# Optimization experiments

Hardware: AMD Instinct MI355X
Metric: run time of the kernel (lower is better)

The kernel has to match this reference:

```python
import jax, jax.numpy as jnp
import numpy as np
import math

B, N, M, Lx = 8, 32, 16, 32
D, TE_DIM, IN_DIM, TT = 64, 16, 17, 63   # hid_dim, te_dim, 1+te_dim, hid_dim-1
H, DH, NL = 4, 16, 2
TAU, DELTA = 60.0, 300.0                 # tau, 5 minutes in seconds
P = B * N * M


def _ln(x, g, b):
    mu = x.mean(-1, keepdims=True)
    v = ((x - mu) ** 2).mean(-1, keepdims=True)
    return (x - mu) / jnp.sqrt(v + 1e-5) * g + b


def _time_bias():
    idx = jnp.arange(M)
    dist = jnp.abs(idx[:, None] - idx[None, :]).astype(jnp.float32) * DELTA
    return jnp.log(jnp.exp(-dist / TAU) + 1e-12)


def _pos_enc():
    pos = jnp.arange(M, dtype=jnp.float32)[:, None]
    div = jnp.exp(jnp.arange(0, D, 2, dtype=jnp.float32) * (-math.log(10000.0) / D))
    pe = jnp.zeros((M, D))
    pe = pe.at[:, 0::2].set(jnp.sin(pos * div))
    pe = pe.at[:, 1::2].set(jnp.cos(pos * div))
    return pe


def _heads(t):   # (b, m, D) -> (b, H, m, DH)
    b, m, _ = t.shape
    return t.reshape(b, m, H, DH).transpose(0, 2, 1, 3)


def _merge(t):   # (b, H, m, DH) -> (b, m, D)
    b, _, m, _ = t.shape
    return t.transpose(0, 2, 1, 3).reshape(b, m, D)


def _patch_gattn(x, pm, qw, qb, kw, kb, vw, vb, ow, ob, tbias):
    q, k, v = _heads(x @ qw.T + qb), _heads(x @ kw.T + kb), _heads(x @ vw.T + vb)
    a = jnp.einsum('bhqd,bhkd->bhqk', q, k) / math.sqrt(DH) + tbias[None, None]
    a = jnp.where((pm == 0.0)[:, None, None, :], -1e9, a)
    out = _merge(jnp.einsum('bhqk,bhkd->bhqd', jax.nn.softmax(a, -1), v))
    return (out @ ow.T + ob) * pm[..., None]


def _mha(q_in, kv_in, in_w, in_b, ow, ob, kpm=None):
    wq, wk, wv = in_w[:D], in_w[D:2 * D], in_w[2 * D:]
    bq, bk, bv = in_b[:D], in_b[D:2 * D], in_b[2 * D:]
    q = _heads(q_in @ wq.T + bq)
    k = _heads(kv_in @ wk.T + bk)
    v = _heads(kv_in @ wv.T + bv)
    a = jnp.einsum('bhqd,bhkd->bhqk', q, k) / math.sqrt(DH)
    if kpm is not None:
        a = jnp.where(kpm[:, None, None, :], -1e9, a)
    out = _merge(jnp.einsum('bhqk,bhkd->bhqd', jax.nn.softmax(a, -1), v))
    return out @ ow.T + ob


def _forward(x, mask, ttcn_w1, ttcn_b1, ttcn_w2, ttcn_b2, ttcn_w3, ttcn_b3, t_bias,
             ga_qw, ga_qb, ga_kw, ga_kb, ga_vw, ga_vb, ga_ow, ga_ob,
             tf_in_w, tf_in_b, tf_out_w, tf_out_b, tf_ln1_g, tf_ln1_b, tf_ln2_g, tf_ln2_b,
             tf_fw1, tf_fb1, tf_fw2, tf_fb2,
             q_embed, cls_in_w, cls_in_b, cls_out_w, cls_out_b, logit_w, logit_b):
    m = mask.astype(x.dtype)                          # (P, Lx, 1)
    # --- TTCN: per-sample dynamic filter generation + masked seq-softmax agg ---
    h = jax.nn.relu(x @ ttcn_w1.T + ttcn_b1)
    h = jax.nn.relu(h @ ttcn_w2.T + ttcn_b2)
    filt = h @ ttcn_w3.T + ttcn_b3                    # (P, Lx, IN_DIM*TT)
    filt = filt * m + (1.0 - m) * (-1e8)
    fs = jax.nn.softmax(filt, axis=1).reshape(P, Lx, TT, IN_DIM)
    h_t = jax.nn.relu(jnp.einsum('pli,plti->pt', x, fs) + t_bias)   # (P, TT)
    mask_patch = (m.sum(axis=1) > 0).astype(x.dtype)  # (P, 1)
    xp = jnp.concatenate([h_t, mask_patch], -1).reshape(B, N, M, D)
    pm = mask_patch.reshape(B, N, M)
    tbias = _time_bias()
    pe = _pos_enc()
    xc = xp
    for l in range(NL):
        if l > 0:
            x_last = xc
        xb = xc.reshape(B * N, M, D)
        pmb = pm.reshape(B * N, M)
        xb = xb + _patch_gattn(xb, pmb, ga_qw[l], ga_qb[l], ga_kw[l], ga_kb[l],
                               ga_vw[l], ga_vb[l], ga_ow[l], ga_ob[l], tbias)
        xb = xb + pe[None]
        # post-norm TransformerEncoderLayer (tf_layer = 1, no attn mask, eval mode)
        attn = _mha(xb, xb, tf_in_w[l], tf_in_b[l], tf_out_w[l], tf_out_b[l])
        xb = _ln(xb + attn, tf_ln1_g[l], tf_ln1_b[l])
        ff = jax.nn.relu(xb @ tf_fw1[l].T + tf_fb1[l]) @ tf_fw2[l].T + tf_fb2[l]
        xb = _ln(xb + ff, tf_ln2_g[l], tf_ln2_b[l])
        xc = xb.reshape(B, N, M, D)
        if l > 0:
            xc = x_last + xc
    x_seq = xc.mean(axis=1)                            # (B, M, D)
    kpm = ~((pm > 0).any(axis=1))                      # (B, M), True = padded
    qs = jnp.broadcast_to(q_embed[None], (B, 5, D))
    z = _mha(qs, x_seq, cls_in_w, cls_in_b, cls_out_w, cls_out_b, kpm=kpm)
    return (z @ logit_w.T + logit_b)[..., 0]           # (B, 5)


def setup_inputs() -> dict:
    key = jax.random.key(0)
    ks = iter(jax.random.split(key, 64))
    def rn(shape, s=0.1):
        return jax.random.normal(next(ks), shape, jnp.float32) * s
    inp = {
        'x': jax.random.normal(next(ks), (P, Lx, IN_DIM), jnp.float32),
        'mask': jax.random.randint(next(ks), (P, Lx, 1), 0, 2, jnp.int32),
        'ttcn_w1': rn((TT, IN_DIM)), 'ttcn_b1': jnp.zeros((TT,)),
        'ttcn_w2': rn((TT, TT)), 'ttcn_b2': jnp.zeros((TT,)),
        'ttcn_w3': rn((IN_DIM * TT, TT)), 'ttcn_b3': jnp.zeros((IN_DIM * TT,)),
        't_bias': rn((1, TT)),
        'ga_qw': rn((NL, D, D)), 'ga_qb': jnp.zeros((NL, D)),
        'ga_kw': rn((NL, D, D)), 'ga_kb': jnp.zeros((NL, D)),
        'ga_vw': rn((NL, D, D)), 'ga_vb': jnp.zeros((NL, D)),
        'ga_ow': rn((NL, D, D)), 'ga_ob': jnp.zeros((NL, D)),
        'tf_in_w': rn((NL, 3 * D, D)), 'tf_in_b': jnp.zeros((NL, 3 * D)),
        'tf_out_w': rn((NL, D, D)), 'tf_out_b': jnp.zeros((NL, D)),
        'tf_ln1_g': jnp.ones((NL, D)), 'tf_ln1_b': jnp.zeros((NL, D)),
        'tf_ln2_g': jnp.ones((NL, D)), 'tf_ln2_b': jnp.zeros((NL, D)),
        'tf_fw1': rn((NL, 2048, D)), 'tf_fb1': jnp.zeros((NL, 2048)),
        'tf_fw2': rn((NL, D, 2048)), 'tf_fb2': jnp.zeros((NL, D)),
        'q_embed': rn((5, D), 1.0),
        'cls_in_w': rn((3 * D, D)), 'cls_in_b': jnp.zeros((3 * D,)),
        'cls_out_w': rn((D, D)), 'cls_out_b': jnp.zeros((D,)),
        'logit_w': rn((1, D)), 'logit_b': jnp.zeros((1,)),
    }
    return inp


def reference(x, mask, ttcn_w1, ttcn_b1, ttcn_w2, ttcn_b2, ttcn_w3, ttcn_b3, t_bias,
              ga_qw, ga_qb, ga_kw, ga_kb, ga_vw, ga_vb, ga_ow, ga_ob,
              tf_in_w, tf_in_b, tf_out_w, tf_out_b, tf_ln1_g, tf_ln1_b, tf_ln2_g, tf_ln2_b,
              tf_fw1, tf_fb1, tf_fw2, tf_fb2,
              q_embed, cls_in_w, cls_in_b, cls_out_w, cls_out_b, logit_w, logit_b):
    return _forward(x, mask, ttcn_w1, ttcn_b1, ttcn_w2, ttcn_b2, ttcn_w3, ttcn_b3, t_bias,
                    ga_qw, ga_qb, ga_kw, ga_kb, ga_vw, ga_vb, ga_ow, ga_ob,
                    tf_in_w, tf_in_b, tf_out_w, tf_out_b, tf_ln1_g, tf_ln1_b, tf_ln2_g, tf_ln2_b,
                    tf_fw1, tf_fb1, tf_fw2, tf_fb2,
                    q_embed, cls_in_w, cls_in_b, cls_out_w, cls_out_b, logit_w, logit_b)
```

## Files before the change

### kernel.cpp

```cpp
#include <hip/hip_runtime.h>
#include <hip/hip_bf16.h>
#include <math.h>

#define B_  8
#define N_  32
#define M_  16
#define LX  32
#define D_  64
#define IN_DIM_ 17
#define TT_ 63
#define H_  4
#define DH_ 16
#define P_TOT 4096
#define BN_ 256
#define FF_ 2048

#define FRAG_TOT 83200
#define OFF_INW  2048
#define OFF_OUTW 3584
#define OFF_FW1  4096
#define OFF_FW2  20480

typedef unsigned short ushort_t;
typedef __attribute__((ext_vector_type(8))) short short8;
typedef __attribute__((ext_vector_type(4))) float floatx4;

#define MFMA16(a,b,c) __builtin_amdgcn_mfma_f32_16x16x32_bf16((a),(b),(c),0,0,0)

__device__ __forceinline__ float fast_exp2(float x){
#if __has_builtin(__builtin_amdgcn_exp2f)
  return __builtin_amdgcn_exp2f(x);
#else
  return __expf(x * 0.6931471805599453f);
#endif
}
__device__ __forceinline__ float fast_rcp(float x){
#if __has_builtin(__builtin_amdgcn_rcpf)
  return __builtin_amdgcn_rcpf(x);
#else
  return 1.0f / x;
#endif
}

__device__ __forceinline__ ushort_t f2bf(float f){
  unsigned u = __float_as_uint(f);
  u += 0x7FFFu + ((u >> 16) & 1u);
  return (ushort_t)(u >> 16);
}
__device__ __forceinline__ float bf2f(ushort_t h){ return __uint_as_float(((unsigned)h) << 16); }

__device__ __forceinline__ uint4 pack8(const ushort_t* h){
  uint4 u;
  u.x = (unsigned)h[0] | ((unsigned)h[1] << 16);
  u.y = (unsigned)h[2] | ((unsigned)h[3] << 16);
  u.z = (unsigned)h[4] | ((unsigned)h[5] << 16);
  u.w = (unsigned)h[6] | ((unsigned)h[7] << 16);
  return u;
}

__device__ __forceinline__ void split8(const float* r, short8& hi, short8& lo){
  #pragma unroll
  for (int j = 0; j < 8; ++j){
    float v = r[j];
    ushort_t h = f2bf(v);
    ushort_t l2 = f2bf(v - bf2f(h));
    hi[j] = (short)h; lo[j] = (short)l2;
  }
}
__device__ __forceinline__ uint4 cvt8(const float* r){
  ushort_t hh[8];
  #pragma unroll
  for (int j = 0; j < 8; ++j) hh[j] = f2bf(r[j]);
  return pack8(hh);
}
__device__ __forceinline__ short8 cvt8s(const float* r){
  union { uint4 u4; short8 s8; } cv;
  cv.u4 = cvt8(r);
  return cv.s8;
}

__device__ __forceinline__ floatx4 mm3(short8 ah, short8 al, short8 bh, short8 bl, floatx4 c){
  c = MFMA16(ah, bh, c); c = MFMA16(ah, bl, c); c = MFMA16(al, bh, c); return c;
}

__device__ __forceinline__ float dot64(const float* __restrict__ a, const float* __restrict__ w){
  const float4* a4 = (const float4*)a;
  const float4* w4 = (const float4*)w;
  float acc = 0.f;
  #pragma unroll
  for (int k = 0; k < 16; ++k){ float4 x = a4[k], y = w4[k];
    acc += x.x*y.x + x.y*y.y + x.z*y.z + x.w*y.w; }
  return acc;
}
__device__ __forceinline__ float dot16(const float* __restrict__ a, const float* __restrict__ b){
  const float4* a4 = (const float4*)a; const float4* b4 = (const float4*)b;
  float acc = 0.f;
  #pragma unroll
  for (int k = 0; k < 4; ++k){ float4 x = a4[k], y = b4[k];
    acc += x.x*y.x + x.y*y.y + x.z*y.z + x.w*y.w; }
  return acc;
}

__device__ __forceinline__ void packA68(const float* buf, short8* fA, int tid){
  if (tid < 128){
    int ln = tid & 63, ks = tid >> 6;
    const float* r = buf + (ln & 15)*68 + ks*32 + ((ln >> 4) & 3)*8;
    short8 hi, lo; split8(r, hi, lo);
    fA[tid] = hi; fA[128 + tid] = lo;
  }
}

__device__ __forceinline__ float wsum64(float v){
  v += __shfl_xor(v, 1, 64);  v += __shfl_xor(v, 2, 64);
  v += __shfl_xor(v, 4, 64);  v += __shfl_xor(v, 8, 64);
  v += __shfl_xor(v, 16, 64); v += __shfl_xor(v, 32, 64);
  return v;
}

__global__ __launch_bounds__(256) void prep_kernel(
    const float* __restrict__ w1, const float* __restrict__ w2, const float* __restrict__ w3,
    const float* __restrict__ gqw, const float* __restrict__ gkw,
    const float* __restrict__ gvw, const float* __restrict__ gow,
    const float* __restrict__ inw, const float* __restrict__ outw,
    const float* __restrict__ fw1, const float* __restrict__ fw2,
    uint4* __restrict__ fr)
{
  int s = blockIdx.x*256 + threadIdx.x;
  if (s >= FRAG_TOT) return;
  const float* src; int Nr, Kr, KS, rel; int w3seg = 0, noLo = 0;
  if (s < 256)      { src = w1; Nr=63;  Kr=17; KS=1; rel = s; noLo = 1; }
  else if (s < 768) { src = w2; Nr=63;  Kr=63; KS=2; rel = s-256; noLo = 1; }
  else if (s < 9472){ src = w3; Nr=1071;Kr=63; KS=2; rel = s-768; w3seg = 1; noLo = 1; }
  else {
    int t = s - 9472, l = t / 36864, r2 = t - l*36864;
    if (r2 < 512)        { src = gqw + l*4096;   Nr=64;  Kr=64;   KS=2;  rel = r2; }
    else if (r2 < 1024)  { src = gkw + l*4096;   Nr=64;  Kr=64;   KS=2;  rel = r2-512; }
    else if (r2 < 1536)  { src = gvw + l*4096;   Nr=64;  Kr=64;   KS=2;  rel = r2-1024; }
    else if (r2 < 2048)  { src = gow + l*4096;   Nr=64;  Kr=64;   KS=2;  rel = r2-1536; }
    else if (r2 < 3584)  { src = inw + l*12288;  Nr=192; Kr=64;   KS=2;  rel = r2-2048; }
    else if (r2 < 4096)  { src = outw + l*4096;  Nr=64;  Kr=64;   KS=2;  rel = r2-3584; }
    else if (r2 < 20480) { src = fw1 + l*131072; Nr=2048;Kr=64;   KS=2;  rel = r2-4096; noLo = 1; }
    else                 { src = fw2 + l*131072; Nr=64;  Kr=2048; KS=64; rel = r2-20480; noLo = 1; }
  }
  int lane = rel & 63, tmp = rel >> 6;
  int ks = tmp % KS, nt = tmp / KS;
  int kb = ks*32 + ((lane >> 4) & 3)*8;
  int n, validn;
  if (w3seg){
    int i = nt >> 2, tq = nt & 3;
    int t = tq*16 + (lane & 15);
    n = t*17 + i;
    validn = (t < 63);
  } else {
    n = nt*16 + (lane & 15);
    validn = (n < Nr);
  }
  float v[8];
  #pragma unroll
  for (int j = 0; j < 8; ++j){
    v[j] = (validn && (kb + j) < Kr) ? src[n*Kr + kb + j] : 0.f;
    if (w3seg){
      if ((kb + j) == 63) v[j] = 1.0f;
      v[j] *= 1.4426950408889634f;
    }
  }
  ushort_t hh[8];
  #pragma unroll
  for (int j = 0; j < 8; ++j) hh[j] = f2bf(v[j]);
  fr[s] = pack8(hh);
  if (!noLo){
    ushort_t ll[8];
    #pragma unroll
    for (int j = 0; j < 8; ++j) ll[j] = f2bf(v[j] - bf2f(hh[j]));
    fr[FRAG_TOT + s] = pack8(ll);
  }
}

__global__ __launch_bounds__(256) void ttcn_kernel(
    const float* __restrict__ x, const int* __restrict__ mask,
    const float* __restrict__ b1, const float* __restrict__ b2,
    const float* __restrict__ tb,
    const short8* __restrict__ w1bhi,
    const short8* __restrict__ w2bhi,
    const short8* __restrict__ w3bhi,
    float* __restrict__ xp, float* __restrict__ pm,
    float* __restrict__ xsws)
{
  __shared__ __align__(16) char pool[16512];
  float*    xs    = (float*)(pool + 0);
  float*    xst   = (float*)(pool + 2560);
  int*      cmap  = (int*)  (pool + 5008);
  float*    xsumv = (float*)(pool + 5136);
  int*      Vp    = (int*)  (pool + 5204);
  short8*   xfhi  = (short8*)(pool + 5216);
  ushort_t* h1t   = (ushort_t*)(pool + 7264);
  ushort_t* h2t   = (ushort_t*)(pool + 11872);

  const int p = blockIdx.x, tid = threadIdx.x;
  const int lane = tid & 63, wvi = tid >> 6;
  const int nidx = lane & 15, quad = lane >> 4;

  if (p < 128 && tid < 64) xsws[p*64 + tid] = 0.f;

  for (int idx = tid; idx < LX*IN_DIM_; idx += 256){
    int l = (idx * 3856) >> 16;
    int i = idx - l*17;
    xs[l*20 + i] = x[p*(LX*IN_DIM_) + idx];
  }
  if (tid < 64){
    int mv = (tid < 32) ? mask[p*LX + tid] : 0;
    unsigned long long bal = __ballot(mv != 0);
    if (tid < 32) cmap[tid] = 0;
    int pos = __popcll(bal & ((1ull << tid) - 1ull));
    if (mv != 0) cmap[pos] = tid;
    if (tid == 0) *Vp = (int)__popcll(bal);
  }
  __syncthreads();
  const int V   = *Vp;
  const int two = (V > 16);

  if (tid < 128){
    int mt = tid >> 6;
    if (mt == 0 || two){
      int lc = cmap[mt*16 + nidx];
      float r[8];
      #pragma unroll
      for (int j = 0; j < 8; ++j){
        int k = quad*8 + j;
        r[j] = (k < IN_DIM_) ? xs[lc*20 + k] : 0.f;
      }
      ((uint4*)xfhi)[tid] = cvt8(r);
    }
  } else {
    if (tid < 128 + IN_DIM_){
      int i = tid - 128;
      float s = 0.f;
      #pragma unroll
      for (int l = 0; l < LX; ++l) s += xs[l*20 + i];
      xsumv[i] = s;
    }
    if (two){
      for (int idx = tid - 128; idx < 544; idx += 128){
        int i = idx >> 5, cl = idx & 31;
        xst[i*36 + cl] = xs[cmap[cl]*20 + i];
      }
    } else {
      for (int idx = tid - 128; idx < 272; idx += 128){
        int i = idx >> 4, cl = idx & 15;
        xst[i*36 + cl] = xs[cmap[cl]*20 + i];
      }
    }
  }
  __syncthreads();

  {
    short8 axh0 = xfhi[lane];
    short8 bh = w1bhi[wvi*64 + lane];
    floatx4 a0 = {0.f,0.f,0.f,0.f};
    a0 = MFMA16(axh0, bh, a0);
    int t = wvi*16 + nidx;
    float bb = (t < TT_) ? b1[t] : 0.f;
    if (two){
      short8 axh1 = xfhi[64 + lane];
      floatx4 a1 = {0.f,0.f,0.f,0.f};
      a1 = MFMA16(axh1, bh, a1);
      #pragma unroll
      for (int r = 0; r < 4; ++r)
        h1t[(16+quad*4+r)*72 + t] = f2bf(fmaxf(a1[r] + bb, 0.f));
    }
    #pragma unroll
    for (int r = 0; r < 4; ++r)
      h1t[(quad*4+r)*72 + t] = f2bf(fmaxf(a0[r] + bb, 0.f));
  }
  __syncthreads();

  {
    short8 bh0 = w2bhi[(wvi*2+0)*64 + lane];
    short8 bh1 = w2bhi[(wvi*2+1)*64 + lane];
    short8 a00 = *(const short8*)((const char*)h1t + (nidx*72 + quad*8)*2);
    short8 a01 = *(const short8*)((const char*)h1t + (nidx*72 + 32 + quad*8)*2);
    floatx4 a0 = {0.f,0.f,0.f,0.f};
    a0 = MFMA16(a00, bh0, a0); a0 = MFMA16(a01, bh1, a0);
    int t = wvi*16 + nidx;
    float bb = (t < TT_) ? b2[t] : 0.f;
    if (two){
      short8 a10 = *(const short8*)((const char*)h1t + ((16+nidx)*72 + quad*8)*2);
      short8 a11 = *(const short8*)((const char*)h1t + ((16+nidx)*72 + 32 + quad*8)*2);
      floatx4 a1 = {0.f,0.f,0.f,0.f};
      a1 = MFMA16(a10, bh0, a1); a1 = MFMA16(a11, bh1, a1);
      #pragma unroll
      for (int r = 0; r < 4; ++r)
        h2t[(16+quad*4+r)*72 + t] = f2bf(fmaxf(a1[r] + bb, 0.f));
    }
    #pragma unroll
    for (int r = 0; r < 4; ++r)
      h2t[(quad*4+r)*72 + t] = f2bf(fmaxf(a0[r] + bb, 0.f));
  }
  __syncthreads();

  {
    short8 ah0[2], ah1[2];
    #pragma unroll
    for (int ks = 0; ks < 2; ++ks)
      ah0[ks] = *(const short8*)((const char*)h2t + (nidx*72 + ks*32 + quad*8)*2);
    if (two){
      #pragma unroll
      for (int ks = 0; ks < 2; ++ks)
        ah1[ks] = *(const short8*)((const char*)h2t + ((16+nidx)*72 + ks*32 + quad*8)*2);
    }
    if (quad == 3){
      if (two) ah1[1][7] = (short)((16 + nidx >= V) ? f2bf(-1e8f) : (ushort_t)0);
      else     ah0[1][7] = (short)((nidx >= V)      ? f2bf(-1e8f) : (ushort_t)0);
    }
    const int t_out = wvi*16 + nidx;
    const int rA = quad*4;
    float acc_t = 0.f;
    if (two){
      #pragma unroll
      for (int it = 0; it < 17; ++it){
        short8 bh0 = w3bhi[((wvi + it*4)*2+0)*64 + lane];
        short8 bh1 = w3bhi[((wvi + it*4)*2+1)*64 + lane];
        floatx4 a0 = {0.f,0.f,0.f,0.f}, a1 = {0.f,0.f,0.f,0.f};
        a0 = MFMA16(ah0[0], bh0, a0); a0 = MFMA16(ah0[1], bh1, a0);
        a1 = MFMA16(ah1[0], bh0, a1); a1 = MFMA16(ah1[1], bh1, a1);

        const float4 xA = *(const float4*)(xst + it*36 + rA);
        const float4 xB = *(const float4*)(xst + it*36 + rA + 16);
        float den0 = 0.f, den1 = 0.f, num0 = 0.f, num1 = 0.f;
        float e;
        e = fast_exp2(a0[0]); den0 += e; num0 = fmaf(e, xA.x, num0);
        e = fast_exp2(a0[1]); den0 += e; num0 = fmaf(e, xA.y, num0);
        e = fast_exp2(a0[2]); den0 += e; num0 = fmaf(e, xA.z, num0);
        e = fast_exp2(a0[3]); den0 += e; num0 = fmaf(e, xA.w, num0);
        e = fast_exp2(a1[0]); den1 += e; num1 = fmaf(e, xB.x, num1);
        e = fast_exp2(a1[1]); den1 += e; num1 = fmaf(e, xB.y, num1);
        e = fast_exp2(a1[2]); den1 += e; num1 = fmaf(e, xB.z, num1);
        e = fast_exp2(a1[3]); den1 += e; num1 = fmaf(e, xB.w, num1);
        float den = den0 + den1, num = num0 + num1;
        den += __shfl_xor(den, 16, 64); den += __shfl_xor(den, 32, 64);
        num += __shfl_xor(num, 16, 64); num += __shfl_xor(num, 32, 64);
        float res = (den > 0.f) ? num * fast_rcp(den) : xsumv[it] * (1.f/32.f);
        acc_t += res;
      }
    } else {
      #pragma unroll
      for (int it = 0; it < 17; ++it){
        short8 bh0 = w3bhi[((wvi + it*4)*2+0)*64 + lane];
        short8 bh1 = w3bhi[((wvi + it*4)*2+1)*64 + lane];
        floatx4 a0 = {0.f,0.f,0.f,0.f};
        a0 = MFMA16(ah0[0], bh0, a0); a0 = MFMA16(ah0[1], bh1, a0);

        const float4 xA = *(const float4*)(xst + it*36 + rA);
        float den = 0.f, num = 0.f, e;
        e = fast_exp2(a0[0]); den += e; num = fmaf(e, xA.x, num);
        e = fast_exp2(a0[1]); den += e; num = fmaf(e, xA.y, num);
        e = fast_exp2(a0[2]); den += e; num = fmaf(e, xA.z, num);
        e = fast_exp2(a0[3]); den += e; num = fmaf(e, xA.w, num);
        den += __shfl_xor(den, 16, 64); den += __shfl_xor(den, 32, 64);
        num += __shfl_xor(num, 16, 64); num += __shfl_xor(num, 32, 64);
        float res = (den > 0.f) ? num * fast_rcp(den) : xsumv[it] * (1.f/32.f);
        acc_t += res;
      }
    }
    if (quad == 0 && t_out < TT_)
      xp[p*D_ + t_out] = fmaxf(acc_t + tb[t_out], 0.f);
  }
  if (tid == 0){
    float mp = (V > 0) ? 1.f : 0.f;
    xp[p*D_ + TT_] = mp;
    pm[p] = mp;
  }
}

__global__ __launch_bounds__(512) void layer12_kernel(
    const float* __restrict__ xin, const float* __restrict__ pm,
    const short8* __restrict__ frS,
    const float* __restrict__ gqb, const float* __restrict__ gkb,
    const float* __restrict__ gvb, const float* __restrict__ gob,
    const float* __restrict__ inb, const float* __restrict__ outb,
    const float* __restrict__ ln1g, const float* __restrict__ ln1b,
    const float* __restrict__ fb1, const float* __restrict__ fb2,
    const float* __restrict__ ln2g, const float* __restrict__ ln2b,
    float* __restrict__ xsws)
{
  __shared__ __align__(16) float xb[16*68];
  __shared__ __align__(16) float xb2[16*68];
  __shared__ __align__(16) float q_[16*68];
  __shared__ __align__(16) float k_[16*68];
  __shared__ __align__(16) float v_[16*68];
  __shared__ __align__(16) float ao[16*68];
  __shared__ __align__(16) float ss[1024];
  __shared__ __align__(16) short8 fragA[256];
  __shared__ __align__(16) float hbuf[8*16*36];
  __shared__ __align__(16) float part[8*16*68];
  __shared__ __align__(16) float pe_t[1024];
  __shared__ float tbt[16];
  __shared__ float pmv[16];

  const int bn = blockIdx.x, tid = threadIdx.x;
  const int lane = tid & 63, wvi = tid >> 6;
  const int nidx = lane & 15, quad = lane >> 4;
  const float* xin_p = xin + bn*1024;

  for (int o = tid; o < 1024; o += 512) xb[(o>>6)*68 + (o&63)] = xin_p[o];
  if (tid < 16) pmv[tid] = pm[bn*16 + tid];
  for (int o = tid; o < 1024; o += 512){
    int tok = o >> 6, d = o & 63;
    float div = __expf((float)(d & ~1) * (-0.14391156831212793f));
    float arg = (float)tok * div;
    pe_t[o] = (d & 1) ? cosf(arg) : sinf(arg);
  }
  if (tid >= 32 && tid < 48) tbt[tid-32] = logf(expf(-5.0f*(float)(tid-32)) + 1e-12f);
  __syncthreads();

  for (int l = 0; l < 2; ++l){
    const int lbase = 9472 + l*36864;
    const float* gqbL = gqb + l*64;  const float* gkbL = gkb + l*64;
    const float* gvbL = gvb + l*64;  const float* gobL = gob + l*64;
    const float* inbL = inb + l*192; const float* outbL = outb + l*64;
    const float* ln1gL = ln1g + l*64; const float* ln1bL = ln1b + l*64;
    const float* fb1L = fb1 + l*2048; const float* fb2L = fb2 + l*64;
    const float* ln2gL = ln2g + l*64; const float* ln2bL = ln2b + l*64;

    float xres[2];
    xres[0] = xb[wvi*68 + lane];
    xres[1] = xb[(wvi+8)*68 + lane];

    short8 gU0[4], gU1[4], mU0[4], mU1[4], ob4[4];
    {
      int b0 = lbase + wvi*128;
      gU0[0] = frS[b0 + lane];       gU0[1] = frS[FRAG_TOT + b0 + lane];
      gU0[2] = frS[b0 + 64 + lane];  gU0[3] = frS[FRAG_TOT + b0 + 64 + lane];
      int m0 = lbase + OFF_INW + wvi*128;
      mU0[0] = frS[m0 + lane];       mU0[1] = frS[FRAG_TOT + m0 + lane];
      mU0[2] = frS[m0 + 64 + lane];  mU0[3] = frS[FRAG_TOT + m0 + 64 + lane];
      if (wvi < 4){
        int b1 = lbase + (wvi+8)*128;
        gU1[0] = frS[b1 + lane];       gU1[1] = frS[FRAG_TOT + b1 + lane];
        gU1[2] = frS[b1 + 64 + lane];  gU1[3] = frS[FRAG_TOT + b1 + 64 + lane];
        int m1 = lbase + OFF_INW + (wvi+8)*128;
        mU1[0] = frS[m1 + lane];       mU1[1] = frS[FRAG_TOT + m1 + lane];
        mU1[2] = frS[m1 + 64 + lane];  mU1[3] = frS[FRAG_TOT + m1 + 64 + lane];
        int bo = lbase + 1536 + wvi*128;
        ob4[0] = frS[bo + lane];       ob4[1] = frS[FRAG_TOT + bo + lane];
        ob4[2] = frS[bo + 64 + lane];  ob4[3] = frS[FRAG_TOT + bo + 64 + lane];
      }
    }

    packA68(xb, fragA, tid);
    __syncthreads();
    {
      short8 axh0 = fragA[lane], axh1 = fragA[64+lane];
      short8 axl0 = fragA[128+lane], axl1 = fragA[192+lane];
      {
        int u = wvi;
        floatx4 c = {0.f,0.f,0.f,0.f};
        c = mm3(axh0, axl0, gU0[0], gU0[1], c);
        c = mm3(axh1, axl1, gU0[2], gU0[3], c);
        int sel = u >> 2, d = (u & 3)*16 + nidx;
        float bb = (sel == 0 ? gqbL : gkbL)[d];
        float* dst = (sel == 0 ? q_ : k_);
        #pragma unroll
        for (int r = 0; r < 4; ++r) dst[(quad*4+r)*68 + d] = c[r] + bb;
      }
      if (wvi < 4){
        int u = wvi + 8;
        floatx4 c = {0.f,0.f,0.f,0.f};
        c = mm3(axh0, axl0, gU1[0], gU1[1], c);
        c = mm3(axh1, axl1, gU1[2], gU1[3], c);
        int d = (u & 3)*16 + nidx;
        float bb = gvbL[d];
        #pragma unroll
        for (int r = 0; r < 4; ++r) v_[(quad*4+r)*68 + d] = c[r] + bb;
      }
    }
    __syncthreads();
    {
      int row = tid >> 3;
      int h = row >> 4, qm = row & 15;
      int km0 = (tid & 7) * 2;
      float s2[2];
      #pragma unroll
      for (int j = 0; j < 2; ++j){
        int km = km0 + j;
        float acc = dot16(q_ + qm*68 + h*16, k_ + km*68 + h*16);
        int dd = qm - km; if (dd < 0) dd = -dd;
        acc = acc * 0.25f + tbt[dd];
        if (pmv[km] == 0.f) acc = -1e9f;
        s2[j] = acc;
      }
      float mx = fmaxf(s2[0], s2[1]);
      mx = fmaxf(mx, __shfl_xor(mx, 1, 64));
      mx = fmaxf(mx, __shfl_xor(mx, 2, 64));
      mx = fmaxf(mx, __shfl_xor(mx, 4, 64));
      float e2[2], se = 0.f;
      #pragma unroll
      for (int j = 0; j < 2; ++j){ e2[j] = __expf(s2[j]-mx); se += e2[j]; }
      se += __shfl_xor(se, 1, 64);
      se += __shfl_xor(se, 2, 64);
      se += __shfl_xor(se, 4, 64);
      float inv = fast_rcp(se);
      #pragma unroll
      for (int j = 0; j < 2; ++j) ss[row*16 + km0 + j] = e2[j]*inv;
    }
    __syncthreads();
    for (int o = tid; o < 1024; o += 512){
      int m = o >> 6, d = o & 63, h = d >> 4;
      float acc = 0.f;
      #pragma unroll
      for (int km = 0; km < 16; ++km) acc += ss[h*256 + m*16 + km] * v_[km*68 + d];
      ao[m*68 + d] = acc;
    }
    __syncthreads();
    packA68(ao, fragA, tid);
    __syncthreads();
    if (wvi < 4){
      short8 axh0 = fragA[lane], axh1 = fragA[64+lane];
      short8 axl0 = fragA[128+lane], axl1 = fragA[192+lane];
      floatx4 c = {0.f,0.f,0.f,0.f};
      c = mm3(axh0, axl0, ob4[0], ob4[1], c);
      c = mm3(axh1, axl1, ob4[2], ob4[3], c);
      int d = wvi*16 + nidx;
      float bb = gobL[d];
      #pragma unroll
      for (int r = 0; r < 4; ++r){
        int tok = quad*4 + r;
        xb[tok*68 + d] += (c[r] + bb) * pmv[tok] + pe_t[tok*64 + d];
      }
    }
    __syncthreads();

    short8 mob[4], f1c[4], f2c[4];
    if (wvi < 4){
      int base = lbase + OFF_OUTW + wvi*128;
      mob[0] = frS[base + lane];       mob[1] = frS[FRAG_TOT + base + lane];
      mob[2] = frS[base + 64 + lane];  mob[3] = frS[FRAG_TOT + base + 64 + lane];
    }
    {
      int f1base = lbase + OFF_FW1, f2base = lbase + OFF_FW2;
      #pragma unroll
      for (int t2 = 0; t2 < 2; ++t2){
        int sb = f1base + ((wvi*16+t2)*2)*64 + lane;
        f1c[t2*2+0] = frS[sb];
        f1c[t2*2+1] = frS[sb + 64];
      }
      #pragma unroll
      for (int ntd = 0; ntd < 4; ++ntd)
        f2c[ntd] = frS[f2base + (ntd*64 + wvi*8)*64 + lane];
    }

    packA68(xb, fragA, tid);
    __syncthreads();
    {
      short8 axh0 = fragA[lane], axh1 = fragA[64+lane];
      short8 axl0 = fragA[128+lane], axl1 = fragA[192+lane];
      {
        int u = wvi;
        floatx4 c = {0.f,0.f,0.f,0.f};
        c = mm3(axh0, axl0, mU0[0], mU0[1], c);
        c = mm3(axh1, axl1, mU0[2], mU0[3], c);
        int sel = u >> 2, d = (u & 3)*16 + nidx;
        float bb = inbL[u*16 + nidx];
        float* dst = (sel == 0 ? q_ : k_);
        #pragma unroll
        for (int r = 0; r < 4; ++r) dst[(quad*4+r)*68 + d] = c[r] + bb;
      }
      if (wvi < 4){
        int u = wvi + 8;
        floatx4 c = {0.f,0.f,0.f,0.f};
        c = mm3(axh0, axl0, mU1[0], mU1[1], c);
        c = mm3(axh1, axl1, mU1[2], mU1[3], c);
        int d = (u & 3)*16 + nidx;
        float bb = inbL[u*16 + nidx];
        #pragma unroll
        for (int r = 0; r < 4; ++r) v_[(quad*4+r)*68 + d] = c[r] + bb;
      }
    }
    __syncthreads();
    {
      int row = tid >> 3;
      int h = row >> 4, qm = row & 15;
      int km0 = (tid & 7) * 2;
      float s2[2];
      #pragma unroll
      for (int j = 0; j < 2; ++j)
        s2[j] = 0.25f * dot16(q_ + qm*68 + h*16, k_ + (km0+j)*68 + h*16);
      float mx = fmaxf(s2[0], s2[1]);
      mx = fmaxf(mx, __shfl_xor(mx, 1, 64));
      mx = fmaxf(mx, __shfl_xor(mx, 2, 64));
      mx = fmaxf(mx, __shfl_xor(mx, 4, 64));
      float e2[2], se = 0.f;
      #pragma unroll
      for (int j = 0; j < 2; ++j){ e2[j] = __expf(s2[j]-mx); se += e2[j]; }
      se += __shfl_xor(se, 1, 64);
      se += __shfl_xor(se, 2, 64);
      se += __shfl_xor(se, 4, 64);
      float inv = fast_rcp(se);
      #pragma unroll
      for (int j = 0; j < 2; ++j) ss[row*16 + km0 + j] = e2[j]*inv;
    }
    __syncthreads();
    for (int o = tid; o < 1024; o += 512){
      int m = o >> 6, d = o & 63, h = d >> 4;
      float acc = 0.f;
      #pragma unroll
      for (int km = 0; km < 16; ++km) acc += ss[h*256 + m*16 + km] * v_[km*68 + d];
      ao[m*68 + d] = acc;
    }
    __syncthreads();
    packA68(ao, fragA, tid);
    __syncthreads();
    if (wvi < 4){
      short8 axh0 = fragA[lane], axh1 = fragA[64+lane];
      short8 axl0 = fragA[128+lane], axl1 = fragA[192+lane];
      floatx4 c = {0.f,0.f,0.f,0.f};
      c = mm3(axh0, axl0, mob[0], mob[1], c);
      c = mm3(axh1, axl1, mob[2], mob[3], c);
      int d = wvi*16 + nidx;
      float bb = outbL[d];
      #pragma unroll
      for (int r = 0; r < 4; ++r) xb[(quad*4+r)*68 + d] += c[r] + bb;
    }
    __syncthreads();

    {
      float a = xb[wvi*68 + lane], b = xb[(wvi+8)*68 + lane];
      float mua = wsum64(a) * (1.f/64.f);
      float mub = wsum64(b) * (1.f/64.f);
      float da = a - mua, db = b - mub;
      float va = wsum64(da*da) * (1.f/64.f);
      float vb = wsum64(db*db) * (1.f/64.f);
      float rva = rsqrtf(va + 1e-5f), rvb = rsqrtf(vb + 1e-5f);
      float g = ln1gL[lane], bia = ln1bL[lane];
      xb2[wvi*68 + lane]     = da*rva*g + bia;
      xb2[(wvi+8)*68 + lane] = db*rvb*g + bia;
    }
    __syncthreads();
    packA68(xb2, fragA, tid);
    __syncthreads();

    {
      const int w = wvi;
      const int f1base = lbase + OFF_FW1, f2base = lbase + OFF_FW2;
      short8 axh0 = fragA[lane], axh1 = fragA[64 + lane];
      floatx4 y0 = {0.f,0.f,0.f,0.f}, y1 = y0, y2 = y0, y3 = y0;
      float* hw = hbuf + w*576;

      short8 f1n[4], f2n[4];
      for (int it = 0; it < 8; ++it){
        int ntA = w*16 + it*2;
        floatx4 hA = {0.f,0.f,0.f,0.f}, hB = hA;
        hA = MFMA16(axh0, f1c[0], hA); hA = MFMA16(axh1, f1c[1], hA);
        hB = MFMA16(axh0, f1c[2], hB); hB = MFMA16(axh1, f1c[3], hB);
        float bbA = fb1L[ntA*16 + nidx], bbB = fb1L[ntA*16 + 16 + nidx];
        #pragma unroll
        for (int r = 0; r < 4; ++r){
          hw[(quad*4+r)*36 + nidx]      = fmaxf(hA[r] + bbA, 0.f);
          hw[(quad*4+r)*36 + 16 + nidx] = fmaxf(hB[r] + bbB, 0.f);
        }
        if (it < 7){
          int ntN = ntA + 2, kstN = w*8 + it + 1;
          #pragma unroll
          for (int t2 = 0; t2 < 2; ++t2){
            int sb = f1base + ((ntN+t2)*2)*64 + lane;
            f1n[t2*2+0] = frS[sb];
            f1n[t2*2+1] = frS[sb + 64];
          }
          #pragma unroll
          for (int ntd = 0; ntd < 4; ++ntd)
            f2n[ntd] = frS[f2base + (ntd*64 + kstN)*64 + lane];
        }
        short8 ah = cvt8s(hw + (lane & 15)*36 + quad*8);
        y0 = MFMA16(ah, f2c[0], y0);
        y1 = MFMA16(ah, f2c[1], y1);
        y2 = MFMA16(ah, f2c[2], y2);
        y3 = MFMA16(ah, f2c[3], y3);
        #pragma unroll
        for (int j = 0; j < 4; ++j){ f1c[j] = f1n[j]; f2c[j] = f2n[j]; }
      }
      #pragma unroll
      for (int r = 0; r < 4; ++r){
        int row = (quad*4 + r)*68;
        part[w*1088 + row + nidx]      = y0[r];
        part[w*1088 + row + 16 + nidx] = y1[r];
        part[w*1088 + row + 32 + nidx] = y2[r];
        part[w*1088 + row + 48 + nidx] = y3[r];
      }
    }
    __syncthreads();
    {
      float ra = xb2[wvi*68 + lane] + fb2L[lane];
      float rb = xb2[(wvi+8)*68 + lane] + fb2L[lane];
      #pragma unroll
      for (int ww = 0; ww < 8; ++ww){
        ra += part[ww*1088 + wvi*68 + lane];
        rb += part[ww*1088 + (wvi+8)*68 + lane];
      }
      float mua = wsum64(ra) * (1.f/64.f);
      float mub = wsum64(rb) * (1.f/64.f);
      float da = ra - mua, db = rb - mub;
      float va = wsum64(da*da) * (1.f/64.f);
      float vb = wsum64(db*db) * (1.f/64.f);
      float rva = rsqrtf(va + 1e-5f), rvb = rsqrtf(vb + 1e-5f);
      float g = ln2gL[lane], bia = ln2bL[lane];
      float vva = da*rva*g + bia;
      float vvb = db*rvb*g + bia;
      if (l == 0){
        xb[wvi*68 + lane]     = vva;
        xb[(wvi+8)*68 + lane] = vvb;
      } else {
        int b = bn >> 5;
        atomicAdd(&xsws[(b*M_ + wvi)*64 + lane],     (vva + xres[0]) * (1.f/32.f));
        atomicAdd(&xsws[(b*M_ + wvi + 8)*64 + lane], (vvb + xres[1]) * (1.f/32.f));
      }
    }
    __syncthreads();
  }
}

__global__ __launch_bounds__(256) void final_kernel(
    const float* __restrict__ xsws, const float* __restrict__ pm,
    const float* __restrict__ q_embed,
    const float* __restrict__ cin_w, const float* __restrict__ cin_b,
    const float* __restrict__ cout_w, const float* __restrict__ cout_b,
    const float* __restrict__ logit_w, const float* __restrict__ logit_b,
    float* __restrict__ out)
{
  const int b = blockIdx.x;
  const int tid = threadIdx.x;
  __shared__ __align__(16) float xs[M_ * D_];
  __shared__ float kpmv[M_];
  __shared__ __align__(16) float qv[5 * D_], kv[M_ * D_], vv[M_ * D_];
  __shared__ float sv[H_ * 5 * M_];
  __shared__ __align__(16) float ao[5 * D_], zv[5 * D_];

  for (int o = tid; o < M_ * D_; o += 256) xs[o] = xsws[b*M_*D_ + o];
  if (tid < M_) {
    float any = 0.f;
    #pragma unroll
    for (int n = 0; n < N_; ++n) any += (pm[(b * N_ + n) * M_ + tid] > 0.f) ? 1.f : 0.f;
    kpmv[tid] = (any > 0.f) ? 0.f : 1.f;
  }
  __syncthreads();

  for (int o = tid; o < 5 * D_; o += 256) {
    int qi = o >> 6, d = o & 63;
    qv[o] = cin_b[d] + dot64(q_embed + qi * D_, cin_w + d * D_);
  }
  for (int o = tid; o < 2 * M_ * D_; o += 256) {
    int sel = o >> 10, r = o & 1023, m = r >> 6, d = r & 63;
    float acc = cin_b[D_ + sel * D_ + d] + dot64(xs + m * D_, cin_w + (D_ + sel * D_ + d) * D_);
    ((sel == 0) ? kv : vv)[r] = acc;
  }
  __syncthreads();

  for (int o = tid; o < H_ * 5 * M_; o += 256) {
    int h = o / 80, r = o % 80, qi = r >> 4, km = r & 15;
    float acc = 0.25f * dot16(qv + qi * D_ + h * DH_, kv + km * D_ + h * DH_);
    if (kpmv[km] != 0.f) acc = -1e9f;
    sv[o] = acc;
  }
  __syncthreads();
  if (tid < H_ * 5) {
    int h = tid / 5, qi = tid % 5;
    float* row = sv + h * 80 + qi * M_;
    float mx = -1e30f;
    #pragma unroll
    for (int km = 0; km < M_; ++km) mx = fmaxf(mx, row[km]);
    float se = 0.f;
    #pragma unroll
    for (int km = 0; km < M_; ++km) { float e = __expf(row[km] - mx); row[km] = e; se += e; }
    float inv = 1.f / se;
    #pragma unroll
    for (int km = 0; km < M_; ++km) row[km] *= inv;
  }
  __syncthreads();
  for (int o = tid; o < 5 * D_; o += 256) {
    int qi = o >> 6, d = o & 63, h = d >> 4;
    float acc = 0.f;
    #pragma unroll
    for (int km = 0; km < M_; ++km) acc += sv[h * 80 + qi * M_ + km] * vv[km * D_ + d];
    ao[o] = acc;
  }
  __syncthreads();
  for (int o = tid; o < 5 * D_; o += 256) {
    int qi = o >> 6, d = o & 63;
    zv[o] = cout_b[d] + dot64(ao + qi * D_, cout_w + d * D_);
  }
  __syncthreads();
  if (tid < 5) {
    float acc = logit_b[0] + dot64(zv + tid * D_, logit_w);
    out[b * 5 + tid] = acc;
  }
}

extern "C" void kernel_launch(void* const* d_in, const int* in_sizes, int n_in,
                              void* d_out, int out_size, void* d_ws, size_t ws_size,
                              hipStream_t stream) {
  const float* x       = (const float*)d_in[0];
  const int*   mask    = (const int*)  d_in[1];
  const float* ttcn_w1 = (const float*)d_in[2];
  const float* ttcn_b1 = (const float*)d_in[3];
  const float* ttcn_w2 = (const float*)d_in[4];
  const float* ttcn_b2 = (const float*)d_in[5];
  const float* ttcn_w3 = (const float*)d_in[6];
  const float* ttcn_b3 = (const float*)d_in[7];
  const float* t_bias  = (const float*)d_in[8];
  const float* ga_qw   = (const float*)d_in[9];
  const float* ga_qb   = (const float*)d_in[10];
  const float* ga_kw   = (const float*)d_in[11];
  const float* ga_kb   = (const float*)d_in[12];
  const float* ga_vw   = (const float*)d_in[13];
  const float* ga_vb   = (const float*)d_in[14];
  const float* ga_ow   = (const float*)d_in[15];
  const float* ga_ob   = (const float*)d_in[16];
  const float* tf_in_w = (const float*)d_in[17];
  const float* tf_in_b = (const float*)d_in[18];
  const float* tf_out_w= (const float*)d_in[19];
  const float* tf_out_b= (const float*)d_in[20];
  const float* tf_ln1g = (const float*)d_in[21];
  const float* tf_ln1b = (const float*)d_in[22];
  const float* tf_ln2g = (const float*)d_in[23];
  const float* tf_ln2b = (const float*)d_in[24];
  const float* tf_fw1  = (const float*)d_in[25];
  const float* tf_fb1  = (const float*)d_in[26];
  const float* tf_fw2  = (const float*)d_in[27];
  const float* tf_fb2  = (const float*)d_in[28];
  const float* q_embed = (const float*)d_in[29];
  const float* cls_in_w  = (const float*)d_in[30];
  const float* cls_in_b  = (const float*)d_in[31];
  const float* cls_out_w = (const float*)d_in[32];
  const float* cls_out_b = (const float*)d_in[33];
  const float* logit_w = (const float*)d_in[34];
  const float* logit_b = (const float*)d_in[35];
  (void)ttcn_b3;

  float* wsf  = (float*)d_ws;
  float* xp   = wsf;
  float* pmb  = wsf + P_TOT * D_;
  uint4* fr   = (uint4*)(pmb + P_TOT);
  float* xsws = (float*)(fr + 2*FRAG_TOT);
  const short8* frS = (const short8*)fr;

  prep_kernel<<<325, 256, 0, stream>>>(ttcn_w1, ttcn_w2, ttcn_w3,
      ga_qw, ga_kw, ga_vw, ga_ow, tf_in_w, tf_out_w, tf_fw1, tf_fw2, fr);

  ttcn_kernel<<<P_TOT, 256, 0, stream>>>(x, mask, ttcn_b1, ttcn_b2, t_bias,
      frS + 0, frS + 256, frS + 768,
      xp, pmb, xsws);

  layer12_kernel<<<BN_, 512, 0, stream>>>(xp, pmb, frS,
      ga_qb, ga_kb, ga_vb, ga_ob, tf_in_b, tf_out_b, tf_ln1g, tf_ln1b,
      tf_fb1, tf_fb2, tf_ln2g, tf_ln2b, xsws);

  final_kernel<<<B_, 256, 0, stream>>>(xsws, pmb, q_embed,
                                       cls_in_w, cls_in_b, cls_out_w, cls_out_b,
                                       logit_w, logit_b, (float*)d_out);
}
```

Measured before the change: 223.7 us.

## Process two patches per TTCN block to share weight fragment loads

Each TTCN block now handles two patches (p and p+2048), so the grid is halved and each MFMA weight fragment for all three layers is loaded once and used for both patches. The third-layer loop also prefetches the next iteration's w3 fragments and merges the one- and two-tile paths into a single loop with conditional second tiles. This cuts redundant global weight loads and per-block setup, but doubles shared memory to about 33 KB, raises register pressure, and leaves fewer blocks for latency hiding.

```diff
diff --git a/kernel.cpp b/kernel.cpp
--- a/kernel.cpp
+++ b/kernel.cpp
@@ -186,189 +186,285 @@
     float* __restrict__ xp, float* __restrict__ pm,
     float* __restrict__ xsws)
 {
-  __shared__ __align__(16) char pool[16512];
-  float*    xs    = (float*)(pool + 0);
-  float*    xst   = (float*)(pool + 2560);
-  int*      cmap  = (int*)  (pool + 5008);
-  float*    xsumv = (float*)(pool + 5136);
-  int*      Vp    = (int*)  (pool + 5204);
-  short8*   xfhi  = (short8*)(pool + 5216);
-  ushort_t* h1t   = (ushort_t*)(pool + 7264);
-  ushort_t* h2t   = (ushort_t*)(pool + 11872);
-
-  const int p = blockIdx.x, tid = threadIdx.x;
+  __shared__ __align__(16) char pool[33024];
+  float*    xs0   = (float*)(pool + 0);
+  float*    xs1   = (float*)(pool + 2560);
+  float*    xst0  = (float*)(pool + 5120);
+  float*    xst1  = (float*)(pool + 7568);
+  int*      cmap0 = (int*)  (pool + 10016);
+  int*      cmap1 = (int*)  (pool + 10144);
+  float*    xsum0 = (float*)(pool + 10272);
+  float*    xsum1 = (float*)(pool + 10344);
+  int*      Vp0   = (int*)  (pool + 10416);
+  int*      Vp1   = (int*)  (pool + 10420);
+  short8*   xfhi0 = (short8*)(pool + 10432);
+  short8*   xfhi1 = (short8*)(pool + 12480);
+  ushort_t* h1t0  = (ushort_t*)(pool + 14528);
+  ushort_t* h1t1  = (ushort_t*)(pool + 19136);
+  ushort_t* h2t0  = (ushort_t*)(pool + 23744);
+  ushort_t* h2t1  = (ushort_t*)(pool + 28352);
+
+  const int p0 = blockIdx.x, p1 = blockIdx.x + 2048, tid = threadIdx.x;
   const int lane = tid & 63, wvi = tid >> 6;
   const int nidx = lane & 15, quad = lane >> 4;
 
-  if (p < 128 && tid < 64) xsws[p*64 + tid] = 0.f;
+  if (p0 < 128 && tid < 64) xsws[p0*64 + tid] = 0.f;
 
   for (int idx = tid; idx < LX*IN_DIM_; idx += 256){
     int l = (idx * 3856) >> 16;
     int i = idx - l*17;
-    xs[l*20 + i] = x[p*(LX*IN_DIM_) + idx];
-  }
-  if (tid < 64){
-    int mv = (tid < 32) ? mask[p*LX + tid] : 0;
+    xs0[l*20 + i] = x[p0*(LX*IN_DIM_) + idx];
+  }
+  for (int idx = tid; idx < LX*IN_DIM_; idx += 256){
+    int l = (idx * 3856) >> 16;
+    int i = idx - l*17;
+    xs1[l*20 + i] = x[p1*(LX*IN_DIM_) + idx];
+  }
+  if (tid < 128){
+    int wv = tid >> 6, ln = tid & 63;
+    int pp = wv ? p1 : p0;
+    int* cm = wv ? cmap1 : cmap0;
+    int* VP = wv ? Vp1 : Vp0;
+    int mv = (ln < 32) ? mask[pp*LX + ln] : 0;
     unsigned long long bal = __ballot(mv != 0);
-    if (tid < 32) cmap[tid] = 0;
-    int pos = __popcll(bal & ((1ull << tid) - 1ull));
-    if (mv != 0) cmap[pos] = tid;
-    if (tid == 0) *Vp = (int)__popcll(bal);
-  }
-  __syncthreads();
-  const int V   = *Vp;
-  const int two = (V > 16);
-
-  if (tid < 128){
-    int mt = tid >> 6;
-    if (mt == 0 || two){
-      int lc = cmap[mt*16 + nidx];
+    if (ln < 32) cm[ln] = 0;
+    int pos = __popcll(bal & ((1ull << ln) - 1ull));
+    if (mv != 0) cm[pos] = ln;
+    if (ln == 0) *VP = (int)__popcll(bal);
+  }
+  __syncthreads();
+  const int V0 = *Vp0, V1 = *Vp1;
+  const int two0 = (V0 > 16), two1 = (V1 > 16);
+
+  {
+    int pp = tid >> 7;
+    int mt = (tid >> 6) & 1;
+    const int* cm = pp ? cmap1 : cmap0;
+    int twoX = pp ? two1 : two0;
+    const float* xsX = pp ? xs1 : xs0;
+    short8* xf = pp ? xfhi1 : xfhi0;
+    if (mt == 0 || twoX){
+      int lc = cm[mt*16 + nidx];
       float r[8];
       #pragma unroll
       for (int j = 0; j < 8; ++j){
         int k = quad*8 + j;
-        r[j] = (k < IN_DIM_) ? xs[lc*20 + k] : 0.f;
-      }
-      ((uint4*)xfhi)[tid] = cvt8(r);
+        r[j] = (k < IN_DIM_) ? xsX[lc*20 + k] : 0.f;
+      }
+      ((uint4*)xf)[tid & 127] = cvt8(r);
+    }
+  }
+  if (tid < IN_DIM_){
+    float s = 0.f;
+    #pragma unroll
+    for (int l = 0; l < LX; ++l) s += xs0[l*20 + tid];
+    xsum0[tid] = s;
+  } else if (tid >= 128 && tid < 128 + IN_DIM_){
+    int i = tid - 128;
+    float s = 0.f;
+    #pragma unroll
+    for (int l = 0; l < LX; ++l) s += xs1[l*20 + i];
+    xsum1[i] = s;
+  }
+  if (two0){
+    for (int idx = tid; idx < 544; idx += 256){
+      int i = idx >> 5, cl = idx & 31;
+      xst0[i*36 + cl] = xs0[cmap0[cl]*20 + i];
     }
   } else {
-    if (tid < 128 + IN_DIM_){
-      int i = tid - 128;
-      float s = 0.f;
-      #pragma unroll
-      for (int l = 0; l < LX; ++l) s += xs[l*20 + i];
-      xsumv[i] = s;
-    }
-    if (two){
-      for (int idx = tid - 128; idx < 544; idx += 128){
-        int i = idx >> 5, cl = idx & 31;
-        xst[i*36 + cl] = xs[cmap[cl]*20 + i];
-      }
-    } else {
-      for (int idx = tid - 128; idx < 272; idx += 128){
-        int i = idx >> 4, cl = idx & 15;
-        xst[i*36 + cl] = xs[cmap[cl]*20 + i];
-      }
+    for (int idx = tid; idx < 272; idx += 256){
+      int i = idx >> 4, cl = idx & 15;
+      xst0[i*36 + cl] = xs0[cmap0[cl]*20 + i];
+    }
+  }
+  if (two1){
+    for (int idx = tid; idx < 544; idx += 256){
+      int i = idx >> 5, cl = idx & 31;
+      xst1[i*36 + cl] = xs1[cmap1[cl]*20 + i];
+    }
+  } else {
+    for (int idx = tid; idx < 272; idx += 256){
+      int i = idx >> 4, cl = idx & 15;
+      xst1[i*36 + cl] = xs1[cmap1[cl]*20 + i];
     }
   }
   __syncthreads();
 
   {
-    short8 axh0 = xfhi[lane];
-    short8 bh = w1bhi[wvi*64 + lane];
-    floatx4 a0 = {0.f,0.f,0.f,0.f};
-    a0 = MFMA16(axh0, bh, a0);
     int t = wvi*16 + nidx;
     float bb = (t < TT_) ? b1[t] : 0.f;
-    if (two){
-      short8 axh1 = xfhi[64 + lane];
-      floatx4 a1 = {0.f,0.f,0.f,0.f};
-      a1 = MFMA16(axh1, bh, a1);
+    short8 bh = w1bhi[wvi*64 + lane];
+    {
+      short8 axh0 = xfhi0[lane];
+      floatx4 a0 = {0.f,0.f,0.f,0.f};
+      a0 = MFMA16(axh0, bh, a0);
+      if (two0){
+        short8 axh1 = xfhi0[64 + lane];
+        floatx4 a1 = {0.f,0.f,0.f,0.f};
+        a1 = MFMA16(axh1, bh, a1);
+        #pragma unroll
+        for (int r = 0; r < 4; ++r)
+          h1t0[(16+quad*4+r)*72 + t] = f2bf(fmaxf(a1[r] + bb, 0.f));
+      }
       #pragma unroll
       for (int r = 0; r < 4; ++r)
-        h1t[(16+quad*4+r)*72 + t] = f2bf(fmaxf(a1[r] + bb, 0.f));
-    }
-    #pragma unroll
-    for (int r = 0; r < 4; ++r)
-      h1t[(quad*4+r)*72 + t] = f2bf(fmaxf(a0[r] + bb, 0.f));
+        h1t0[(quad*4+r)*72 + t] = f2bf(fmaxf(a0[r] + bb, 0.f));
+    }
+    {
+      short8 axh0 = xfhi1[lane];
+      floatx4 a0 = {0.f,0.f,0.f,0.f};
+      a0 = MFMA16(axh0, bh, a0);
+      if (two1){
+        short8 axh1 = xfhi1[64 + lane];
+        floatx4 a1 = {0.f,0.f,0.f,0.f};
+        a1 = MFMA16(axh1, bh, a1);
+        #pragma unroll
+        for (int r = 0; r < 4; ++r)
+          h1t1[(16+quad*4+r)*72 + t] = f2bf(fmaxf(a1[r] + bb, 0.f));
+      }
+      #pragma unroll
+      for (int r = 0; r < 4; ++r)
+        h1t1[(quad*4+r)*72 + t] = f2bf(fmaxf(a0[r] + bb, 0.f));
+    }
   }
   __syncthreads();
 
   {
+    int t = wvi*16 + nidx;
+    float bb = (t < TT_) ? b2[t] : 0.f;
     short8 bh0 = w2bhi[(wvi*2+0)*64 + lane];
     short8 bh1 = w2bhi[(wvi*2+1)*64 + lane];
-    short8 a00 = *(const short8*)((const char*)h1t + (nidx*72 + quad*8)*2);
-    short8 a01 = *(const short8*)((const char*)h1t + (nidx*72 + 32 + quad*8)*2);
-    floatx4 a0 = {0.f,0.f,0.f,0.f};
-    a0 = MFMA16(a00, bh0, a0); a0 = MFMA16(a01, bh1, a0);
-    int t = wvi*16 + nidx;
-    float bb = (t < TT_) ? b2[t] : 0.f;
-    if (two){
-      short8 a10 = *(const short8*)((const char*)h1t + ((16+nidx)*72 + quad*8)*2);
-      short8 a11 = *(const short8*)((const char*)h1t + ((16+nidx)*72 + 32 + quad*8)*2);
-      floatx4 a1 = {0.f,0.f,0.f,0.f};
-      a1 = MFMA16(a10, bh0, a1); a1 = MFMA16(a11, bh1, a1);
+    {
+      short8 a00 = *(const short8*)((const char*)h1t0 + (nidx*72 + quad*8)*2);
+      short8 a01 = *(const short8*)((const char*)h1t0 + (nidx*72 + 32 + quad*8)*2);
+      floatx4 a0 = {0.f,0.f,0.f,0.f};
+      a0 = MFMA16(a00, bh0, a0); a0 = MFMA16(a01, bh1, a0);
+      if (two0){
+        short8 a10 = *(const short8*)((const char*)h1t0 + ((16+nidx)*72 + quad*8)*2);
+        short8 a11 = *(const short8*)((const char*)h1t0 + ((16+nidx)*72 + 32 + quad*8)*2);
+        floatx4 a1 = {0.f,0.f,0.f,0.f};
+        a1 = MFMA16(a10, bh0, a1); a1 = MFMA16(a11, bh1, a1);
+        #pragma unroll
+        for (int r = 0; r < 4; ++r)
+          h2t0[(16+quad*4+r)*72 + t] = f2bf(fmaxf(a1[r] + bb, 0.f));
+      }
       #pragma unroll
       for (int r = 0; r < 4; ++r)
-        h2t[(16+quad*4+r)*72 + t] = f2bf(fmaxf(a1[r] + bb, 0.f));
-    }
+        h2t0[(quad*4+r)*72 + t] = f2bf(fmaxf(a0[r] + bb, 0.f));
+    }
+    {
+      short8 a00 = *(const short8*)((const char*)h1t1 + (nidx*72 + quad*8)*2);
+      short8 a01 = *(const short8*)((const char*)h1t1 + (nidx*72 + 32 + quad*8)*2);
+      floatx4 a0 = {0.f,0.f,0.f,0.f};
+      a0 = MFMA16(a00, bh0, a0); a0 = MFMA16(a01, bh1, a0);
+      if (two1){
+        short8 a10 = *(const short8*)((const char*)h1t1 + ((16+nidx)*72 + quad*8)*2);
+        short8 a11 = *(const short8*)((const char*)h1t1 + ((16+nidx)*72 + 32 + quad*8)*2);
+        floatx4 a1 = {0.f,0.f,0.f,0.f};
+        a1 = MFMA16(a10, bh0, a1); a1 = MFMA16(a11, bh1, a1);
+        #pragma unroll
+        for (int r = 0; r < 4; ++r)
+          h2t1[(16+quad*4+r)*72 + t] = f2bf(fmaxf(a1[r] + bb, 0.f));
+      }
+      #pragma unroll
+      for (int r = 0; r < 4; ++r)
+        h2t1[(quad*4+r)*72 + t] = f2bf(fmaxf(a0[r] + bb, 0.f));
+    }
+  }
+  __syncthreads();
+
+  {
+    short8 ahA[2], ahB[2], ahC[2], ahD[2];
     #pragma unroll
-    for (int r = 0; r < 4; ++r)
-      h2t[(quad*4+r)*72 + t] = f2bf(fmaxf(a0[r] + bb, 0.f));
-  }
-  __syncthreads();
-
-  {
-    short8 ah0[2], ah1[2];
-    #pragma unroll
-    for (int ks = 0; ks < 2; ++ks)
-      ah0[ks] = *(const short8*)((const char*)h2t + (nidx*72 + ks*32 + quad*8)*2);
-    if (two){
+    for (int ks = 0; ks < 2; ++ks){
+      ahA[ks] = *(const short8*)((const char*)h2t0 + (nidx*72 + ks*32 + quad*8)*2);
+      ahC[ks] = *(const short8*)((const char*)h2t1 + (nidx*72 + ks*32 + quad*8)*2);
+    }
+    if (two0){
       #pragma unroll
       for (int ks = 0; ks < 2; ++ks)
-        ah1[ks] = *(const short8*)((const char*)h2t + ((16+nidx)*72 + ks*32 + quad*8)*2);
+        ahB[ks] = *(const short8*)((const char*)h2t0 + ((16+nidx)*72 + ks*32 + quad*8)*2);
+    }
+    if (two1){
+      #pragma unroll
+      for (int ks = 0; ks < 2; ++ks)
+        ahD[ks] = *(const short8*)((const char*)h2t1 + ((16+nidx)*72 + ks*32 + quad*8)*2);
     }
     if (quad == 3){
-      if (two) ah1[1][7] = (short)((16 + nidx >= V) ? f2bf(-1e8f) : (ushort_t)0);
-      else     ah0[1][7] = (short)((nidx >= V)      ? f2bf(-1e8f) : (ushort_t)0);
+      if (two0) ahB[1][7] = (short)((16 + nidx >= V0) ? f2bf(-1e8f) : (ushort_t)0);
+      else      ahA[1][7] = (short)((nidx >= V0)      ? f2bf(-1e8f) : (ushort_t)0);
+      if (two1) ahD[1][7] = (short)((16 + nidx >= V1) ? f2bf(-1e8f) : (ushort_t)0);
+      else      ahC[1][7] = (short)((nidx >= V1)      ? f2bf(-1e8f) : (ushort_t)0);
     }
     const int t_out = wvi*16 + nidx;
     const int rA = quad*4;
-    float acc_t = 0.f;
-    if (two){
-      #pragma unroll
-      for (int it = 0; it < 17; ++it){
-        short8 bh0 = w3bhi[((wvi + it*4)*2+0)*64 + lane];
-        short8 bh1 = w3bhi[((wvi + it*4)*2+1)*64 + lane];
-        floatx4 a0 = {0.f,0.f,0.f,0.f}, a1 = {0.f,0.f,0.f,0.f};
-        a0 = MFMA16(ah0[0], bh0, a0); a0 = MFMA16(ah0[1], bh1, a0);
-        a1 = MFMA16(ah1[0], bh0, a1); a1 = MFMA16(ah1[1], bh1, a1);
-
-        const float4 xA = *(const float4*)(xst + it*36 + rA);
-        const float4 xB = *(const float4*)(xst + it*36 + rA + 16);
-        float den0 = 0.f, den1 = 0.f, num0 = 0.f, num1 = 0.f;
-        float e;
-        e = fast_exp2(a0[0]); den0 += e; num0 = fmaf(e, xA.x, num0);
-        e = fast_exp2(a0[1]); den0 += e; num0 = fmaf(e, xA.y, num0);
-        e = fast_exp2(a0[2]); den0 += e; num0 = fmaf(e, xA.z, num0);
-        e = fast_exp2(a0[3]); den0 += e; num0 = fmaf(e, xA.w, num0);
-        e = fast_exp2(a1[0]); den1 += e; num1 = fmaf(e, xB.x, num1);
-        e = fast_exp2(a1[1]); den1 += e; num1 = fmaf(e, xB.y, num1);
-        e = fast_exp2(a1[2]); den1 += e; num1 = fmaf(e, xB.z, num1);
-        e = fast_exp2(a1[3]); den1 += e; num1 = fmaf(e, xB.w, num1);
-        float den = den0 + den1, num = num0 + num1;
-        den += __shfl_xor(den, 16, 64); den += __shfl_xor(den, 32, 64);
-        num += __shfl_xor(num, 16, 64); num += __shfl_xor(num, 32, 64);
-        float res = (den > 0.f) ? num * fast_rcp(den) : xsumv[it] * (1.f/32.f);
-        acc_t += res;
-      }
-    } else {
-      #pragma unroll
-      for (int it = 0; it < 17; ++it){
-        short8 bh0 = w3bhi[((wvi + it*4)*2+0)*64 + lane];
-        short8 bh1 = w3bhi[((wvi + it*4)*2+1)*64 + lane];
+    float accA = 0.f, accB = 0.f;
+    short8 nbh0 = w3bhi[(wvi*2+0)*64 + lane];
+    short8 nbh1 = w3bhi[(wvi*2+1)*64 + lane];
+    for (int it = 0; it < 17; ++it){
+      short8 bh0 = nbh0, bh1 = nbh1;
+      if (it < 16){
+        int nt = wvi + it*4 + 4;
+        nbh0 = w3bhi[(nt*2+0)*64 + lane];
+        nbh1 = w3bhi[(nt*2+1)*64 + lane];
+      }
+      {
         floatx4 a0 = {0.f,0.f,0.f,0.f};
-        a0 = MFMA16(ah0[0], bh0, a0); a0 = MFMA16(ah0[1], bh1, a0);
-
-        const float4 xA = *(const float4*)(xst + it*36 + rA);
+        a0 = MFMA16(ahA[0], bh0, a0); a0 = MFMA16(ahA[1], bh1, a0);
+        const float4 xA = *(const float4*)(xst0 + it*36 + rA);
         float den = 0.f, num = 0.f, e;
         e = fast_exp2(a0[0]); den += e; num = fmaf(e, xA.x, num);
         e = fast_exp2(a0[1]); den += e; num = fmaf(e, xA.y, num);
         e = fast_exp2(a0[2]); den += e; num = fmaf(e, xA.z, num);
         e = fast_exp2(a0[3]); den += e; num = fmaf(e, xA.w, num);
+        if (two0){
+          floatx4 a1 = {0.f,0.f,0.f,0.f};
+          a1 = MFMA16(ahB[0], bh0, a1); a1 = MFMA16(ahB[1], bh1, a1);
+          const float4 xB = *(const float4*)(xst0 + it*36 + rA + 16);
+          e = fast_exp2(a1[0]); den += e; num = fmaf(e, xB.x, num);
+          e = fast_exp2(a1[1]); den += e; num = fmaf(e, xB.y, num);
+          e = fast_exp2(a1[2]); den += e; num = fmaf(e, xB.z, num);
+          e = fast_exp2(a1[3]); den += e; num = fmaf(e, xB.w, num);
+        }
         den += __shfl_xor(den, 16, 64); den += __shfl_xor(den, 32, 64);
         num += __shfl_xor(num, 16, 64); num += __shfl_xor(num, 32, 64);
-        float res = (den > 0.f) ? num * fast_rcp(den) : xsumv[it] * (1.f/32.f);
-        acc_t += res;
-      }
-    }
-    if (quad == 0 && t_out < TT_)
-      xp[p*D_ + t_out] = fmaxf(acc_t + tb[t_out], 0.f);
+        float res = (den > 0.f) ? num * fast_rcp(den) : xsum0[it] * (1.f/32.f);
+        accA += res;
+      }
+      {
+        floatx4 a0 = {0.f,0.f,0.f,0.f};
+        a0 = MFMA16(ahC[0], bh0, a0); a0 = MFMA16(ahC[1], bh1, a0);
+        const float4 xA = *(const float4*)(xst1 + it*36 + rA);
+        float den = 0.f, num = 0.f, e;
+        e = fast_exp2(a0[0]); den += e; num = fmaf(e, xA.x, num);
+        e = fast_exp2(a0[1]); den += e; num = fmaf(e, xA.y, num);
+        e = fast_exp2(a0[2]); den += e; num = fmaf(e, xA.z, num);
+        e = fast_exp2(a0[3]); den += e; num = fmaf(e, xA.w, num);
+        if (two1){
+          floatx4 a1 = {0.f,0.f,0.f,0.f};
+          a1 = MFMA16(ahD[0], bh0, a1); a1 = MFMA16(ahD[1], bh1, a1);
+          const float4 xB = *(const float4*)(xst1 + it*36 + rA + 16);
+          e = fast_exp2(a1[0]); den += e; num = fmaf(e, xB.x, num);
+          e = fast_exp2(a1[1]); den += e; num = fmaf(e, xB.y, num);
+          e = fast_exp2(a1[2]); den += e; num = fmaf(e, xB.z, num);
+          e = fast_exp2(a1[3]); den += e; num = fmaf(e, xB.w, num);
+        }
+        den += __shfl_xor(den, 16, 64); den += __shfl_xor(den, 32, 64);
+        num += __shfl_xor(num, 16, 64); num += __shfl_xor(num, 32, 64);
+        float res = (den > 0.f) ? num * fast_rcp(den) : xsum1[it] * (1.f/32.f);
+        accB += res;
+      }
+    }
+    if (quad == 0 && t_out < TT_){
+      xp[p0*D_ + t_out] = fmaxf(accA + tb[t_out], 0.f);
+      xp[p1*D_ + t_out] = fmaxf(accB + tb[t_out], 0.f);
+    }
   }
   if (tid == 0){
-    float mp = (V > 0) ? 1.f : 0.f;
-    xp[p*D_ + TT_] = mp;
-    pm[p] = mp;
+    float mp0 = (V0 > 0) ? 1.f : 0.f;
+    float mp1 = (V1 > 0) ? 1.f : 0.f;
+    xp[p0*D_ + TT_] = mp0; pm[p0] = mp0;
+    xp[p1*D_ + TT_] = mp1; pm[p1] = mp1;
   }
 }
 
@@ -845,7 +941,7 @@
   prep_kernel<<<325, 256, 0, stream>>>(ttcn_w1, ttcn_w2, ttcn_w3,
       ga_qw, ga_kw, ga_vw, ga_ow, tf_in_w, tf_out_w, tf_fw1, tf_fw2, fr);
 
-  ttcn_kernel<<<P_TOT, 256, 0, stream>>>(x, mask, ttcn_b1, ttcn_b2, t_bias,
+  ttcn_kernel<<<P_TOT/2, 256, 0, stream>>>(x, mask, ttcn_b1, ttcn_b2, t_bias,
       frS + 0, frS + 256, frS + 768,
       xp, pmb, xsws);
 
```

Result: slower. 231.9 us (+3.6%).
